# Kernel tuning notes

Hardware: AMD Instinct MI355X
Metric: run time of the kernel (lower is better)

The kernel has to match this reference:

```python
import jax, jax.numpy as jnp
import numpy as np

B, L, D, V = 2048, 32, 256, 100000  # batch, sentence length, embed dim, vocab
KW = 3  # kernel_width (forced to 3 by the module's shape arithmetic)


def conv_h(x, w, b):
    """1-channel conv over the seq axis, kernel (3,1), pad 2 -> length L+2. x:(B,L,D), w:(3,)."""
    xp = jnp.pad(x, ((0, 0), (2, 2), (0, 0)))
    L_out = x.shape[1] + 2
    out = w[0] * xp[:, 0:L_out] + w[1] * xp[:, 1:L_out + 1] + w[2] * xp[:, 2:L_out + 2]
    return out + b


def avgpool3(x):
    """avg_pool2d kernel (3,1) stride 1 along seq axis. (B,L+2,D) -> (B,L,D)."""
    return (x[:, :-2] + x[:, 1:-1] + x[:, 2:]) / 3.0


def conv3d_21(x, w, b):
    """Conv3d kernel (2,3,1), pad (0,2,0). x:(B,2,L,D), w:(2,3) -> (B,L+2,D)."""
    xp = jnp.pad(x, ((0, 0), (0, 0), (2, 2), (0, 0)))
    L_out = x.shape[2] + 2
    out = jnp.zeros((x.shape[0], L_out, x.shape[3]), dtype=x.dtype)
    for d0 in range(2):
        for k in range(3):
            out = out + w[d0, k] * xp[:, d0, k:k + L_out]
    return out + b


def euclid_attention(a, b):
    """A[k,i,j] = 1/(1 + ||a[k,i]-b[k,j]||_2), computed via the matmul cdist trick."""
    a2 = jnp.sum(a * a, axis=-1)  # (B,La)
    b2 = jnp.sum(b * b, axis=-1)  # (B,Lb)
    d2 = a2[:, :, None] + b2[:, None, :] - 2.0 * jnp.einsum('bid,bjd->bij', a, b)
    d = jnp.sqrt(jnp.maximum(d2, 0.0))
    return 1.0 / (1.0 + d)


def setup_inputs() -> dict:
    key = jax.random.key(0)
    ks = jax.random.split(key, 16)
    inp = {
        'sentence1': jax.random.randint(ks[0], (B, L), 0, V),
        'sentence2': jax.random.randint(ks[1], (B, L), 0, V),
        'embed': jax.random.normal(ks[2], (V, D), dtype=jnp.float32) * 0.05,
        'c1w': jax.random.normal(ks[3], (KW,), dtype=jnp.float32) * 0.3,
        'c1b': jax.random.normal(ks[4], (), dtype=jnp.float32) * 0.05,
        'c2w': jax.random.normal(ks[5], (KW,), dtype=jnp.float32) * 0.3,
        'c2b': jax.random.normal(ks[6], (), dtype=jnp.float32) * 0.05,
        'c3w': jax.random.normal(ks[7], (2, KW), dtype=jnp.float32) * 0.3,
        'c3b': jax.random.normal(ks[8], (), dtype=jnp.float32) * 0.05,
        'W0': jax.random.normal(ks[9], (L, D), dtype=jnp.float32),
        'W1': jax.random.normal(ks[10], (L, D), dtype=jnp.float32),
        'fw1': jax.random.normal(ks[11], (2 * D, 64), dtype=jnp.float32) * 0.05,
        'fb1': jnp.zeros((64,), dtype=jnp.float32),
        'fw2': jax.random.normal(ks[12], (64, 2), dtype=jnp.float32) * 0.1,
        'fb2': jnp.zeros((2,), dtype=jnp.float32),
    }
    return inp


def reference(sentence1, sentence2, embed, c1w, c1b, c2w, c2b, c3w, c3b, W0, W1, fw1, fb1, fw2, fb2):
    e1 = embed[sentence1]                      # (B,L,D)
    e2 = embed[sentence2]
    rep1 = avgpool3(conv_h(e1, c1w, c1b))      # (B,L,D)
    rep2 = avgpool3(conv_h(e2, c1w, c1b))
    A1 = euclid_attention(rep1, rep2)          # (B,L,L)
    att1 = jnp.einsum('bij,jd->bid', A1, W0)   # (B,L,D)
    att2 = jnp.einsum('bij,jd->bid', A1, W1)
    c1 = conv3d_21(jnp.stack([rep1, att1], axis=1), c3w, c3b)  # (B,L+2,D)
    c2 = conv3d_21(jnp.stack([rep2, att2], axis=1), c3w, c3b)
    A2 = euclid_attention(c1, c2)              # (B,L+2,L+2)
    col = jnp.sum(A2, axis=2)                  # (B,L+2)
    row = jnp.sum(A2, axis=1)
    ca1 = avgpool3(c1 * col[:, :, None])       # (B,L,D)
    ca2 = avgpool3(c2 * row[:, :, None])
    v1 = jnp.mean(conv_h(ca1, c2w, c2b), axis=1)  # (B,D)
    v2 = jnp.mean(conv_h(ca2, c2w, c2b), axis=1)
    h = jnp.tanh(jnp.concatenate([v1, v2], axis=1) @ fw1 + fb1)
    logits = h @ fw2 + fb2                     # (B,2)
    return jax.nn.softmax(logits, axis=0)      # faithful: original Softmax(dim=0)
```

## Files before the change

kernel.cpp:

```cpp
#include <hip/hip_runtime.h>
#include <math.h>

#define NB 2048
#define LL 32
#define DD 256
#define LP 34
#define SRH 264
#define SA 35
#define BMS 40

typedef unsigned short u16;
typedef short bf8 __attribute__((ext_vector_type(8)));
typedef float f32x4 __attribute__((ext_vector_type(4)));
typedef float vf2 __attribute__((ext_vector_type(2)));

__device__ __forceinline__ float bfu(u16 h) { return __uint_as_float(((unsigned)h) << 16); }
__device__ __forceinline__ float bf_lo(unsigned u) { return __uint_as_float(u << 16); }
__device__ __forceinline__ float bf_hi(unsigned u) { return __uint_as_float(u & 0xffff0000u); }
__device__ __forceinline__ u16 f2bf(float f) {
    unsigned u = __float_as_uint(f);
    u += 0x7fffu + ((u >> 16) & 1u);
    return (u16)(u >> 16);
}
__device__ __forceinline__ unsigned cvt_pk_bf(float lo, float hi) {
    unsigned r;
    asm("v_cvt_pk_bf16_f32 %0, %1, %2" : "=v"(r) : "v"(lo), "v"(hi));
    return r;
}

__device__ __forceinline__ f32x4 gram8(const u16* __restrict__ A, const u16* __restrict__ B) {
    f32x4 acc = {0.f, 0.f, 0.f, 0.f};
    #pragma unroll
    for (int ks = 0; ks < 8; ++ks) {
        const bf8 a = *(const bf8*)(A + ks * 32);
        const bf8 b = *(const bf8*)(B + ks * 32);
        acc = __builtin_amdgcn_mfma_f32_16x16x32_bf16(a, b, acc, 0, 0, 0);
    }
    return acc;
}

__device__ static const signed char TB2[8][4] = {
    {0,0,1,0}, {0,0,1,16}, {0,16,1,0}, {0,16,1,16},
    {0,0,0,0}, {0,16,0,16}, {1,0,1,0}, {1,16,1,16}};

__device__ static const signed char TB5[15][4] = {
    {0,0,0,0}, {0,16,0,16}, {0,18,0,18}, {1,0,1,0}, {1,16,1,16}, {1,18,1,18},
    {0,0,1,0},  {0,0,1,16},  {0,0,1,18},
    {0,16,1,0}, {0,16,1,16}, {0,16,1,18},
    {0,18,1,0}, {0,18,1,16}, {0,18,1,18}};

__global__ __launch_bounds__(256)
void pack_w(const float* __restrict__ W0, const float* __restrict__ W1, u16* __restrict__ wp)
{
    const int t = blockIdx.x * 256 + threadIdx.x;
    const int lane = t & 63, nt = (t >> 6) & 15, wsel = t >> 10;
    const float* W = wsel ? W1 : W0;
    const int col = nt * 16 + (lane & 15);
    const int k0 = (lane >> 4) * 8;
    unsigned d[4];
    #pragma unroll
    for (int q = 0; q < 4; ++q) {
        const u16 lo = f2bf(W[(size_t)(k0 + 2 * q) * DD + col]);
        const u16 hi = f2bf(W[(size_t)(k0 + 2 * q + 1) * DD + col]);
        d[q] = (unsigned)lo | ((unsigned)hi << 16);
    }
    uint4 u; u.x = d[0]; u.y = d[1]; u.z = d[2]; u.w = d[3];
    ((uint4*)wp)[t] = u;
}

__global__ __launch_bounds__(256, 3)
void abcnn_fused(const int* __restrict__ s1, const int* __restrict__ s2,
                 const float* __restrict__ embed,
                 const float* __restrict__ c1w, const float* __restrict__ c1b,
                 const float* __restrict__ c2w, const float* __restrict__ c2b,
                 const float* __restrict__ c3w, const float* __restrict__ c3b,
                 const float* __restrict__ fw1, const float* __restrict__ fb1,
                 const float* __restrict__ fw2, const float* __restrict__ fb2,
                 const u16* __restrict__ wpack, float* __restrict__ lgts)
{
    __shared__ __align__(16) u16 RC[2][LP][SRH];
    __shared__ float AU[LP * SA];
    __shared__ __align__(16) u16 Bm[LP][BMS];
    __shared__ float nrm[2][LP];
    __shared__ float UN[900];

    const int b    = blockIdx.x;
    const int tid  = threadIdx.x;
    const int lane = tid & 63;
    const int wv   = tid >> 6;
    const int c15  = lane & 15;
    const int q4x  = (lane >> 4) * 4;
    const int ko   = (lane >> 4) * 8;

    {
        const float w0 = c1w[0], w1 = c1w[1], w2 = c1w[2], bb = c1b[0];
        const float gm2 = w0 * (1.f/3.f);
        const float gm1 = (w0 + w1) * (1.f/3.f);
        const float g0  = (w0 + w1 + w2) * (1.f/3.f);
        const float gp1 = (w1 + w2) * (1.f/3.f);
        const float gp2 = w2 * (1.f/3.f);
        const int s  = tid >> 7;
        const int dp = tid & 127;
        const int* sent = (s ? s2 : s1) + b * LL;
        vf2 rep[LL];
        #pragma unroll
        for (int j = 0; j < LL; ++j) rep[j] = (vf2){bb, bb};
        #pragma unroll
        for (int jj = 0; jj < LL; ++jj) {
            const int idx = sent[jj];
            const vf2 x = *(const vf2*)(embed + (size_t)idx * DD + 2 * dp);
            if (jj >= 2)      rep[jj - 2] += gp2 * x;
            if (jj >= 1)      rep[jj - 1] += gp1 * x;
                              rep[jj    ] += g0  * x;
            if (jj <= LL - 2) rep[jj + 1] += gm1 * x;
            if (jj <= LL - 3) rep[jj + 2] += gm2 * x;
        }
        #pragma unroll
        for (int j = 0; j < LL; ++j)
            *(unsigned*)&RC[s][j][2 * dp] = cvt_pk_bf(rep[j].x, rep[j].y);
    }
    __syncthreads();

    {
        f32x4 h2[2];
        #pragma unroll
        for (int k = 0; k < 2; ++k) {
            const int t  = wv * 2 + k;
            const int sa = TB2[t][0], oa = TB2[t][1], sb = TB2[t][2], ob = TB2[t][3];
            const f32x4 G = gram8(&RC[sa][oa + c15][ko], &RC[sb][ob + c15][ko]);
            h2[k] = G;
            if (t >= 4 && (c15 >> 2) == (lane >> 4)) {
                const int r = c15 & 3;
                const float dv = (r == 0) ? G[0] : (r == 1) ? G[1] : (r == 2) ? G[2] : G[3];
                nrm[sa][oa + c15] = dv;
            }
        }
        __syncthreads();
        #pragma unroll
        for (int k = 0; k < 2; ++k) {
            const int t = wv * 2 + k;
            if (t < 4) {
                const int oa = TB2[t][1], ob = TB2[t][3];
                const f32x4 G = h2[k];
                #pragma unroll
                for (int r = 0; r < 4; ++r) {
                    const int i = oa + q4x + r, j = ob + c15;
                    const float d2 = nrm[0][i] + nrm[1][j] - 2.f * G[r];
                    AU[i * SA + j] = 1.f / (1.f + sqrtf(fmaxf(d2, 0.f)));
                }
            }
        }
    }
    __syncthreads();

    {
        const float cw10 = c3w[3], cw11 = c3w[4], cw12 = c3w[5];
        for (int e = tid; e < LP * 32; e += 256) {
            const int i = e >> 5, m = e & 31;
            float acc = 0.f;
            if (i >= 2)           acc += cw10 * AU[(i - 2) * SA + m];
            if (i >= 1 && i < 33) acc += cw11 * AU[(i - 1) * SA + m];
            if (i < 32)           acc += cw12 * AU[i * SA + m];
            Bm[i][m] = f2bf(acc);
        }
    }
    __syncthreads();

    {
        const float cw00 = c3w[0], cw01 = c3w[1], cw02 = c3w[2], cb3 = c3b[0];
        for (int wsel = 0; wsel < 2; ++wsel) {
            f32x4 acc[12];
            #pragma unroll
            for (int k = 0; k < 12; ++k) {
                const int t  = wv + 4 * k;
                const int rq = t >> 4;
                const int ro = (rq == 0) ? 0 : (rq == 1) ? 16 : 18;
                const int n  = t & 15;
                const bf8 a = *(const bf8*)&Bm[ro + c15][ko];
                const bf8 w = *(const bf8*)(wpack + (size_t)((wsel * 16 + n) * 64 + lane) * 8);
                const f32x4 z = {0.f, 0.f, 0.f, 0.f};
                acc[k] = __builtin_amdgcn_mfma_f32_16x16x32_bf16(a, w, z, 0, 0, 0);
                const int d  = n * 16 + c15;
                const int i0 = ro + q4x;
                float tt[6];
                #pragma unroll
                for (int q2 = 0; q2 < 6; ++q2) {
                    const int rr = i0 - 2 + q2;
                    tt[q2] = (rr >= 0 && rr < LL) ? bfu(RC[wsel][rr][d]) : 0.f;
                }
                #pragma unroll
                for (int r = 0; r < 4; ++r)
                    acc[k][r] += cb3 + cw00 * tt[r] + cw01 * tt[r + 1] + cw02 * tt[r + 2];
            }
            __syncthreads();
            #pragma unroll
            for (int k = 0; k < 12; ++k) {
                const int t  = wv + 4 * k;
                const int rq = t >> 4;
                const int ro = (rq == 0) ? 0 : (rq == 1) ? 16 : 18;
                const int n  = t & 15;
                const int d  = n * 16 + c15;
                const int i0 = ro + q4x;
                const unsigned p01 = cvt_pk_bf(acc[k][0], acc[k][1]);
                const unsigned p23 = cvt_pk_bf(acc[k][2], acc[k][3]);
                RC[wsel][i0    ][d] = (u16)p01;
                RC[wsel][i0 + 1][d] = (u16)(p01 >> 16);
                RC[wsel][i0 + 2][d] = (u16)p23;
                RC[wsel][i0 + 3][d] = (u16)(p23 >> 16);
            }
            __syncthreads();
        }
    }

    {
        f32x4 h5[4];
        #pragma unroll
        for (int k = 0; k < 4; ++k) {
            const int t = wv + 4 * k;
            if (t < 15) {
                const int sa = TB5[t][0], oa = TB5[t][1], sb = TB5[t][2], ob = TB5[t][3];
                const f32x4 G = gram8(&RC[sa][oa + c15][ko], &RC[sb][ob + c15][ko]);
                h5[k] = G;
                if (t < 6 && (c15 >> 2) == (lane >> 4)) {
                    const int r = c15 & 3;
                    const float dv = (r == 0) ? G[0] : (r == 1) ? G[1] : (r == 2) ? G[2] : G[3];
                    nrm[sa][oa + c15] = dv;
                }
            }
        }
        __syncthreads();
        #pragma unroll
        for (int k = 0; k < 4; ++k) {
            const int t = wv + 4 * k;
            if (t >= 6 && t < 15) {
                const int oa = TB5[t][1], ob = TB5[t][3];
                const f32x4 G = h5[k];
                #pragma unroll
                for (int r = 0; r < 4; ++r) {
                    const int i = oa + q4x + r, j = ob + c15;
                    const float d2 = nrm[0][i] + nrm[1][j] - 2.f * G[r];
                    AU[i * SA + j] = 1.f / (1.f + sqrtf(fmaxf(d2, 0.f)));
                }
            }
        }
    }
    __syncthreads();

    {
        const float S2 = c2w[0] + c2w[1] + c2w[2];
        const float sc = S2 * (1.f / 102.f);
        if (tid < 68) {
            const bool isCol = tid < 34;
            const int p = isCol ? tid : tid - 34;
            float s = 0.f;
            for (int q = 0; q < LP; ++q) s += AU[isCol ? (p * SA + q) : (q * SA + p)];
            const float cnt = (p == 0 || p == 33) ? 1.f : ((p == 1 || p == 32) ? 2.f : 3.f);
            UN[tid] = s * cnt * sc;
        }
    }
    __syncthreads();

    {
        const float cb2 = c2b[0];
        float v1 = cb2, v2 = cb2;
        #pragma unroll
        for (int p = 0; p < LP; ++p) {
            v1 += UN[p]      * bfu(RC[0][p][tid]);
            v2 += UN[34 + p] * bfu(RC[1][p][tid]);
        }
        UN[68 + tid]       = v1;
        UN[68 + 256 + tid] = v2;
    }
    __syncthreads();

    {
        const int u = tid & 63, sg = tid >> 6;
        const float* vv = &UN[68];
        const float* fp = fw1 + (size_t)(sg * 128) * 64 + u;
        float part = 0.f;
        for (int t = 0; t < 128; ++t) part += vv[sg * 128 + t] * fp[(size_t)t * 64];
        UN[580 + tid] = part;
    }
    __syncthreads();
    if (tid < 64) {
        const float hsum = UN[580 + tid] + UN[644 + tid] + UN[708 + tid] + UN[772 + tid] + fb1[tid];
        UN[836 + tid] = tanhf(hsum);
    }
    __syncthreads();
    if (tid < 2) {
        float lg = fb2[tid];
        for (int u2 = 0; u2 < 64; ++u2) lg += UN[836 + u2] * fw2[u2 * 2 + tid];
        lgts[tid * NB + b] = lg;
    }
}

__global__ __launch_bounds__(1024)
void softmax_dim0(const float* __restrict__ lgts, float* __restrict__ out)
{
    __shared__ float red[17];
    const int tid = threadIdx.x;
    for (int c = 0; c < 2; ++c) {
        const float x0 = lgts[c * NB + tid];
        const float x1 = lgts[c * NB + 1024 + tid];
        float m = fmaxf(x0, x1);
        #pragma unroll
        for (int off = 32; off >= 1; off >>= 1) m = fmaxf(m, __shfl_xor(m, off));
        if ((tid & 63) == 0) red[tid >> 6] = m;
        __syncthreads();
        if (tid == 0) { float t = red[0]; for (int i = 1; i < 16; ++i) t = fmaxf(t, red[i]); red[16] = t; }
        __syncthreads();
        m = red[16];
        const float e0 = expf(x0 - m), e1 = expf(x1 - m);
        float s = e0 + e1;
        #pragma unroll
        for (int off = 32; off >= 1; off >>= 1) s += __shfl_xor(s, off);
        if ((tid & 63) == 0) red[tid >> 6] = s;
        __syncthreads();
        if (tid == 0) { float t = 0.f; for (int i = 0; i < 16; ++i) t += red[i]; red[16] = t; }
        __syncthreads();
        const float inv = 1.f / red[16];
        out[(size_t)tid * 2 + c]          = e0 * inv;
        out[(size_t)(1024 + tid) * 2 + c] = e1 * inv;
        __syncthreads();
    }
}

extern "C" void kernel_launch(void* const* d_in, const int* in_sizes, int n_in,
                              void* d_out, int out_size, void* d_ws, size_t ws_size,
                              hipStream_t stream)
{
    (void)in_sizes; (void)n_in; (void)out_size; (void)ws_size;
    const int*   s1  = (const int*)  d_in[0];
    const int*   s2  = (const int*)  d_in[1];
    const float* emb = (const float*)d_in[2];
    const float* c1w = (const float*)d_in[3];
    const float* c1b = (const float*)d_in[4];
    const float* c2w = (const float*)d_in[5];
    const float* c2b = (const float*)d_in[6];
    const float* c3w = (const float*)d_in[7];
    const float* c3b = (const float*)d_in[8];
    const float* W0  = (const float*)d_in[9];
    const float* W1  = (const float*)d_in[10];
    const float* fw1 = (const float*)d_in[11];
    const float* fb1 = (const float*)d_in[12];
    const float* fw2 = (const float*)d_in[13];
    const float* fb2 = (const float*)d_in[14];
    u16*   wpack = (u16*)d_ws;
    float* lgts  = (float*)((char*)d_ws + 32768);
    float* out   = (float*)d_out;

    pack_w<<<dim3(8), dim3(256), 0, stream>>>(W0, W1, wpack);
    abcnn_fused<<<dim3(NB), dim3(256), 0, stream>>>(s1, s2, emb, c1w, c1b, c2w, c2b,
                                                    c3w, c3b, fw1, fb1, fw2, fb2,
                                                    wpack, lgts);
    softmax_dim0<<<dim3(1), dim3(1024), 0, stream>>>(lgts, out);
}
```

Before: 81.63 us.

## Cut LDS and registers to fit four blocks per CU, build conv3d A-fragments in registers

Shrinks shared memory per block by dropping the Bm and UN buffers. The conv3d A operand is now built directly into registers from AU, and the scalar scratch reuses AU. The embedding conv is rewritten to load a 20-row sliding window per half, replacing the 32-entry accumulator array, which lowers register pressure. Launch bounds rise to 4 blocks per CU, the MFMA tile order is remapped so each wave reuses its A fragment, and s_setprio is added around the MFMA sections. The aim is higher occupancy and fewer LDS round trips and barriers, at the risk of register spills under the tighter bound and redundant AU reads per wave.

```diff
diff --git a/kernel.cpp b/kernel.cpp
--- a/kernel.cpp
+++ b/kernel.cpp
@@ -7,7 +7,6 @@
 #define LP 34
 #define SRH 264
 #define SA 35
-#define BMS 40
 
 typedef unsigned short u16;
 typedef short bf8 __attribute__((ext_vector_type(8)));
@@ -15,8 +14,6 @@
 typedef float vf2 __attribute__((ext_vector_type(2)));
 
 __device__ __forceinline__ float bfu(u16 h) { return __uint_as_float(((unsigned)h) << 16); }
-__device__ __forceinline__ float bf_lo(unsigned u) { return __uint_as_float(u << 16); }
-__device__ __forceinline__ float bf_hi(unsigned u) { return __uint_as_float(u & 0xffff0000u); }
 __device__ __forceinline__ u16 f2bf(float f) {
     unsigned u = __float_as_uint(f);
     u += 0x7fffu + ((u >> 16) & 1u);
@@ -68,7 +65,7 @@
     ((uint4*)wp)[t] = u;
 }
 
-__global__ __launch_bounds__(256, 3)
+__global__ __launch_bounds__(256, 4)
 void abcnn_fused(const int* __restrict__ s1, const int* __restrict__ s2,
                  const float* __restrict__ embed,
                  const float* __restrict__ c1w, const float* __restrict__ c1b,
@@ -80,9 +77,7 @@
 {
     __shared__ __align__(16) u16 RC[2][LP][SRH];
     __shared__ float AU[LP * SA];
-    __shared__ __align__(16) u16 Bm[LP][BMS];
     __shared__ float nrm[2][LP];
-    __shared__ float UN[900];
 
     const int b    = blockIdx.x;
     const int tid  = threadIdx.x;
@@ -102,27 +97,35 @@
         const int s  = tid >> 7;
         const int dp = tid & 127;
         const int* sent = (s ? s2 : s1) + b * LL;
-        vf2 rep[LL];
-        #pragma unroll
-        for (int j = 0; j < LL; ++j) rep[j] = (vf2){bb, bb};
-        #pragma unroll
-        for (int jj = 0; jj < LL; ++jj) {
-            const int idx = sent[jj];
-            const vf2 x = *(const vf2*)(embed + (size_t)idx * DD + 2 * dp);
-            if (jj >= 2)      rep[jj - 2] += gp2 * x;
-            if (jj >= 1)      rep[jj - 1] += gp1 * x;
-                              rep[jj    ] += g0  * x;
-            if (jj <= LL - 2) rep[jj + 1] += gm1 * x;
-            if (jj <= LL - 3) rep[jj + 2] += gm2 * x;
-        }
-        #pragma unroll
-        for (int j = 0; j < LL; ++j)
-            *(unsigned*)&RC[s][j][2 * dp] = cvt_pk_bf(rep[j].x, rep[j].y);
+        #pragma unroll
+        for (int half = 0; half < 2; ++half) {
+            const int j0 = half * 16;
+            vf2 x[20];
+            #pragma unroll
+            for (int i = 0; i < 20; ++i) {
+                const int rr = j0 - 2 + i;
+                if (rr >= 0 && rr < LL)
+                    x[i] = *(const vf2*)(embed + (size_t)sent[rr] * DD + 2 * dp);
+                else
+                    x[i] = (vf2){0.f, 0.f};
+            }
+            #pragma unroll
+            for (int j = 0; j < 16; ++j) {
+                vf2 acc = {bb, bb};
+                acc += gm2 * x[j];
+                acc += gm1 * x[j + 1];
+                acc += g0  * x[j + 2];
+                acc += gp1 * x[j + 3];
+                acc += gp2 * x[j + 4];
+                *(unsigned*)&RC[s][j0 + j][2 * dp] = cvt_pk_bf(acc.x, acc.y);
+            }
+        }
     }
     __syncthreads();
 
     {
         f32x4 h2[2];
+        __builtin_amdgcn_s_setprio(1);
         #pragma unroll
         for (int k = 0; k < 2; ++k) {
             const int t  = wv * 2 + k;
@@ -135,6 +138,7 @@
                 nrm[sa][oa + c15] = dv;
             }
         }
+        __builtin_amdgcn_s_setprio(0);
         __syncthreads();
         #pragma unroll
         for (int k = 0; k < 2; ++k) {
@@ -155,58 +159,68 @@
 
     {
         const float cw10 = c3w[3], cw11 = c3w[4], cw12 = c3w[5];
-        for (int e = tid; e < LP * 32; e += 256) {
-            const int i = e >> 5, m = e & 31;
-            float acc = 0.f;
-            if (i >= 2)           acc += cw10 * AU[(i - 2) * SA + m];
-            if (i >= 1 && i < 33) acc += cw11 * AU[(i - 1) * SA + m];
-            if (i < 32)           acc += cw12 * AU[i * SA + m];
-            Bm[i][m] = f2bf(acc);
-        }
-    }
-    __syncthreads();
-
-    {
         const float cw00 = c3w[0], cw01 = c3w[1], cw02 = c3w[2], cb3 = c3b[0];
+        bf8 afr[3];
+        #pragma unroll
+        for (int rq = 0; rq < 3; ++rq) {
+            const int ro = (rq == 0) ? 0 : (rq == 1) ? 16 : 18;
+            const int i = ro + c15;
+            unsigned pk[4];
+            #pragma unroll
+            for (int p = 0; p < 4; ++p) {
+                float e[2];
+                #pragma unroll
+                for (int hh = 0; hh < 2; ++hh) {
+                    const int m = ko + 2 * p + hh;
+                    float acc = 0.f;
+                    if (i >= 2)           acc += cw10 * AU[(i - 2) * SA + m];
+                    if (i >= 1 && i < 33) acc += cw11 * AU[(i - 1) * SA + m];
+                    if (i < 32)           acc += cw12 * AU[i * SA + m];
+                    e[hh] = acc;
+                }
+                pk[p] = cvt_pk_bf(e[0], e[1]);
+            }
+            afr[rq] = *(bf8*)&pk[0];
+        }
         for (int wsel = 0; wsel < 2; ++wsel) {
             f32x4 acc[12];
+            __builtin_amdgcn_s_setprio(1);
             #pragma unroll
             for (int k = 0; k < 12; ++k) {
-                const int t  = wv + 4 * k;
-                const int rq = t >> 4;
+                const int rq = k >> 2;
                 const int ro = (rq == 0) ? 0 : (rq == 1) ? 16 : 18;
-                const int n  = t & 15;
-                const bf8 a = *(const bf8*)&Bm[ro + c15][ko];
+                const int n  = wv + 4 * (k & 3);
                 const bf8 w = *(const bf8*)(wpack + (size_t)((wsel * 16 + n) * 64 + lane) * 8);
                 const f32x4 z = {0.f, 0.f, 0.f, 0.f};
-                acc[k] = __builtin_amdgcn_mfma_f32_16x16x32_bf16(a, w, z, 0, 0, 0);
-                const int d  = n * 16 + c15;
+                f32x4 d = __builtin_amdgcn_mfma_f32_16x16x32_bf16(afr[rq], w, z, 0, 0, 0);
+                const int dcol = n * 16 + c15;
                 const int i0 = ro + q4x;
                 float tt[6];
                 #pragma unroll
                 for (int q2 = 0; q2 < 6; ++q2) {
                     const int rr = i0 - 2 + q2;
-                    tt[q2] = (rr >= 0 && rr < LL) ? bfu(RC[wsel][rr][d]) : 0.f;
+                    tt[q2] = (rr >= 0 && rr < LL) ? bfu(RC[wsel][rr][dcol]) : 0.f;
                 }
                 #pragma unroll
                 for (int r = 0; r < 4; ++r)
-                    acc[k][r] += cb3 + cw00 * tt[r] + cw01 * tt[r + 1] + cw02 * tt[r + 2];
-            }
+                    d[r] += cb3 + cw00 * tt[r] + cw01 * tt[r + 1] + cw02 * tt[r + 2];
+                acc[k] = d;
+            }
+            __builtin_amdgcn_s_setprio(0);
             __syncthreads();
             #pragma unroll
             for (int k = 0; k < 12; ++k) {
-                const int t  = wv + 4 * k;
-                const int rq = t >> 4;
+                const int rq = k >> 2;
                 const int ro = (rq == 0) ? 0 : (rq == 1) ? 16 : 18;
-                const int n  = t & 15;
-                const int d  = n * 16 + c15;
+                const int n  = wv + 4 * (k & 3);
+                const int dcol = n * 16 + c15;
                 const int i0 = ro + q4x;
                 const unsigned p01 = cvt_pk_bf(acc[k][0], acc[k][1]);
                 const unsigned p23 = cvt_pk_bf(acc[k][2], acc[k][3]);
-                RC[wsel][i0    ][d] = (u16)p01;
-                RC[wsel][i0 + 1][d] = (u16)(p01 >> 16);
-                RC[wsel][i0 + 2][d] = (u16)p23;
-                RC[wsel][i0 + 3][d] = (u16)(p23 >> 16);
+                RC[wsel][i0    ][dcol] = (u16)p01;
+                RC[wsel][i0 + 1][dcol] = (u16)(p01 >> 16);
+                RC[wsel][i0 + 2][dcol] = (u16)p23;
+                RC[wsel][i0 + 3][dcol] = (u16)(p23 >> 16);
             }
             __syncthreads();
         }
@@ -214,6 +228,7 @@
 
     {
         f32x4 h5[4];
+        __builtin_amdgcn_s_setprio(1);
         #pragma unroll
         for (int k = 0; k < 4; ++k) {
             const int t = wv + 4 * k;
@@ -228,6 +243,7 @@
                 }
             }
         }
+        __builtin_amdgcn_s_setprio(0);
         __syncthreads();
         #pragma unroll
         for (int k = 0; k < 4; ++k) {
@@ -249,14 +265,17 @@
     {
         const float S2 = c2w[0] + c2w[1] + c2w[2];
         const float sc = S2 * (1.f / 102.f);
+        float p6 = 0.f;
         if (tid < 68) {
             const bool isCol = tid < 34;
             const int p = isCol ? tid : tid - 34;
-            float s = 0.f;
-            for (int q = 0; q < LP; ++q) s += AU[isCol ? (p * SA + q) : (q * SA + p)];
+            float ssum = 0.f;
+            for (int q = 0; q < LP; ++q) ssum += AU[isCol ? (p * SA + q) : (q * SA + p)];
             const float cnt = (p == 0 || p == 33) ? 1.f : ((p == 1 || p == 32) ? 2.f : 3.f);
-            UN[tid] = s * cnt * sc;
-        }
+            p6 = ssum * cnt * sc;
+        }
+        __syncthreads();
+        if (tid < 68) AU[tid] = p6;
     }
     __syncthreads();
 
@@ -265,31 +284,31 @@
         float v1 = cb2, v2 = cb2;
         #pragma unroll
         for (int p = 0; p < LP; ++p) {
-            v1 += UN[p]      * bfu(RC[0][p][tid]);
-            v2 += UN[34 + p] * bfu(RC[1][p][tid]);
-        }
-        UN[68 + tid]       = v1;
-        UN[68 + 256 + tid] = v2;
+            v1 += AU[p]      * bfu(RC[0][p][tid]);
+            v2 += AU[34 + p] * bfu(RC[1][p][tid]);
+        }
+        AU[68 + tid]       = v1;
+        AU[68 + 256 + tid] = v2;
     }
     __syncthreads();
 
     {
         const int u = tid & 63, sg = tid >> 6;
-        const float* vv = &UN[68];
+        const float* vv = &AU[68];
         const float* fp = fw1 + (size_t)(sg * 128) * 64 + u;
         float part = 0.f;
         for (int t = 0; t < 128; ++t) part += vv[sg * 128 + t] * fp[(size_t)t * 64];
-        UN[580 + tid] = part;
+        AU[580 + tid] = part;
     }
     __syncthreads();
     if (tid < 64) {
-        const float hsum = UN[580 + tid] + UN[644 + tid] + UN[708 + tid] + UN[772 + tid] + fb1[tid];
-        UN[836 + tid] = tanhf(hsum);
+        const float hsum = AU[580 + tid] + AU[644 + tid] + AU[708 + tid] + AU[772 + tid] + fb1[tid];
+        AU[836 + tid] = tanhf(hsum);
     }
     __syncthreads();
     if (tid < 2) {
         float lg = fb2[tid];
-        for (int u2 = 0; u2 < 64; ++u2) lg += UN[836 + u2] * fw2[u2 * 2 + tid];
+        for (int u2 = 0; u2 < 64; ++u2) lg += AU[836 + u2] * fw2[u2 * 2 + tid];
         lgts[tid * NB + b] = lg;
     }
 }
@@ -339,12 +358,12 @@
     const float* c2b = (const float*)d_in[6];
     const float* c3w = (const float*)d_in[7];
     const float* c3b = (const float*)d_in[8];
-    const float* W0  = (const float*)d_in[9];
-    const float* W1  = (const float*)d_in[10];
     const float* fw1 = (const float*)d_in[11];
     const float* fb1 = (const float*)d_in[12];
     const float* fw2 = (const float*)d_in[13];
     const float* fb2 = (const float*)d_in[14];
+    const float* W0  = (const float*)d_in[9];
+    const float* W1  = (const float*)d_in[10];
     u16*   wpack = (u16*)d_ws;
     float* lgts  = (float*)((char*)d_ws + 32768);
     float* out   = (float*)d_out;
```

New measurement: 76.89 us. -5.8%, faster.
